# Performance work log

Measured on AMD Instinct MI355X. Metric: run time of the kernel, lower is better.

Reference implementation:

```python
import jax, jax.numpy as jnp
import numpy as np

B, V, D = 8, 1024, 512
H = 8
HD = D // H
MAX_HOP = 8


def setup_inputs() -> dict:
    key = jax.random.key(0)
    ks = jax.random.split(key, 5)
    x = jax.random.normal(ks[0], (B, V, D), dtype=jnp.float32)
    w_qkv = jax.random.normal(ks[1], (D, 3 * D), dtype=jnp.float32) * (D ** -0.5)
    w_out = jax.random.normal(ks[2], (D, D), dtype=jnp.float32) * (D ** -0.5)
    b_out = jnp.zeros((D,), dtype=jnp.float32)
    rpe_bias = jax.random.normal(ks[3], (H, MAX_HOP + 1), dtype=jnp.float32) * 0.02
    hop_matrix = jax.random.randint(ks[4], (V, V), 0, MAX_HOP + 1, dtype=jnp.int32)
    return {"x": x, "w_qkv": w_qkv, "w_out": w_out, "b_out": b_out,
            "rpe_bias": rpe_bias, "hop_matrix": hop_matrix}


def reference(x, w_qkv, w_out, b_out, rpe_bias, hop_matrix):
    b, v, d = x.shape
    scale = HD ** -0.5
    qkv = x @ w_qkv                                   # [B, V, 3D]
    q, k, val = jnp.split(qkv, 3, axis=-1)
    # [B, V, D] -> [B, H, V, HD]
    def split_heads(t):
        return t.reshape(b, v, H, HD).transpose(0, 2, 1, 3)
    q, k, val = split_heads(q), split_heads(k), split_heads(val)
    scores = jnp.einsum('bhvd,bhwd->bhvw', q, k)      # [B, H, V, V]
    bias = rpe_bias[:, hop_matrix]                    # gather -> [H, V, V]
    attn = jax.nn.softmax((scores + bias[None]) * scale, axis=-1)
    out_heads = jnp.einsum('bhvw,bhwd->bhvd', attn, val)
    out = out_heads.transpose(0, 2, 1, 3).reshape(b, v, d)
    out = out @ w_out + b_out
    return out, attn
```

## Files before the change

### kernel.cpp

```cpp
#include <hip/hip_runtime.h>

typedef __attribute__((ext_vector_type(8))) short bf16x8;
typedef __attribute__((ext_vector_type(4))) float f32x4;

#define MFMA16(A,B,C) __builtin_amdgcn_mfma_f32_16x16x32_bf16(A,B,C,0,0,0)

typedef const __attribute__((address_space(1))) void gas_t;
typedef __attribute__((address_space(3))) void las_t;
#define GLOAD16(g, l) __builtin_amdgcn_global_load_lds((gas_t*)(g), (las_t*)(l), 16, 0, 0)

__device__ __forceinline__ unsigned short f2bf(float f){
  unsigned int u = __float_as_uint(f);
  u += 0x7FFFu + ((u >> 16) & 1u);
  return (unsigned short)(u >> 16);
}
__device__ __forceinline__ float bf2f(unsigned short s){
  return __uint_as_float(((unsigned int)s) << 16);
}
__device__ __forceinline__ int swz(int row, int kbyte){
  return (row * 128 + kbyte) ^ ((row & 7) << 4);
}

__global__ __launch_bounds__(256) void k_prep(
    const float* __restrict__ w_qkv, const float* __restrict__ w_out,
    const float* __restrict__ x,
    const int* __restrict__ hop, const float* __restrict__ rpe_bias,
    unsigned short* __restrict__ wqT, unsigned short* __restrict__ woT,
    unsigned short* __restrict__ xb, unsigned short* __restrict__ biasT)
{
  __shared__ float tile[64][65];
  __shared__ float rl[72];
  const int bid = blockIdx.x, tid = threadIdx.x;
  if (bid < 256) {
    const float* src; unsigned short* dst; int srcld, kq0, n0;
    if (bid < 192) {
      int tn = bid >> 3, tk = bid & 7;
      src = w_qkv; dst = wqT; srcld = 1536; kq0 = tk * 64; n0 = tn * 64;
    } else {
      int j = bid - 192; int tn = j >> 3, tk = j & 7;
      src = w_out; dst = woT; srcld = 512; kq0 = tk * 64; n0 = tn * 64;
    }
    const int c = tid & 63, r4 = tid >> 6;
#pragma unroll
    for (int i = 0; i < 16; ++i) {
      int rr = r4 * 16 + i;
      tile[rr][c] = src[(size_t)(kq0 + rr) * srcld + n0 + c];
    }
    __syncthreads();
#pragma unroll
    for (int i = 0; i < 16; ++i) {
      int rr = r4 * 16 + i;
      dst[(size_t)(n0 + rr) * 512 + kq0 + c] = f2bf(tile[c][rr]);
    }
  } else if (bid < 1280) {
    int base = (bid - 256) * 1024 + tid;
#pragma unroll
    for (int i = 0; i < 4; ++i) {
      int j = base + i * 256;
      float4 xv = *reinterpret_cast<const float4*>(x + (size_t)j * 4);
      ushort4 o;
      o.x = f2bf(xv.x); o.y = f2bf(xv.y); o.z = f2bf(xv.z); o.w = f2bf(xv.w);
      *reinterpret_cast<ushort4*>(xb + (size_t)j * 4) = o;
    }
  } else {
    if (tid < 72) rl[tid] = rpe_bias[tid];
    __syncthreads();
    int j = (bid - 1280) * 256 + tid;
    int hv = hop[j];
#pragma unroll
    for (int h = 0; h < 8; ++h)
      biasT[((size_t)h << 20) + j] = f2bf(rl[h * 9 + hv]);
  }
}

__global__ __launch_bounds__(256) void k_qkv(
    const unsigned short* __restrict__ xb, const unsigned short* __restrict__ wqT,
    unsigned short* __restrict__ q, unsigned short* __restrict__ k_,
    unsigned short* __restrict__ valT)
{
  __shared__ char lds[32768];
  char* At = lds; char* Bt = lds + 16384;
  const int tid = threadIdx.x;
  const int wid = tid >> 6, lane = tid & 63, g = lane >> 4, r = lane & 15;
  const int wm = wid >> 1, wn = wid & 1;
  const int m0 = blockIdx.x * 128, n0 = blockIdx.y * 128;
  const int l8 = lane >> 3;
  const int colel = ((lane & 7) ^ l8) * 8;

  f32x4 acc[4][4];
#pragma unroll
  for (int a = 0; a < 4; ++a)
#pragma unroll
    for (int b = 0; b < 4; ++b) acc[a][b] = (f32x4){0.f, 0.f, 0.f, 0.f};

  for (int kt = 0; kt < 8; ++kt) {
    const int k0 = kt * 64;
    __syncthreads();
#pragma unroll
    for (int i = 0; i < 4; ++i) {
      int row = wid * 32 + i * 8 + l8;
      GLOAD16(xb  + (size_t)(m0 + row) * 512 + k0 + colel, At + wid * 4096 + i * 1024);
      GLOAD16(wqT + (size_t)(n0 + row) * 512 + k0 + colel, Bt + wid * 4096 + i * 1024);
    }
    __syncthreads();
#pragma unroll
    for (int kk = 0; kk < 2; ++kk) {
      bf16x8 af[4], bf[4];
      const int kb = (kk * 32 + 8 * g) * 2;
#pragma unroll
      for (int mi = 0; mi < 4; ++mi)
        af[mi] = *reinterpret_cast<const bf16x8*>(At + swz(wm * 64 + mi * 16 + r, kb));
#pragma unroll
      for (int ni = 0; ni < 4; ++ni)
        bf[ni] = *reinterpret_cast<const bf16x8*>(Bt + swz(wn * 64 + ni * 16 + r, kb));
#pragma unroll
      for (int mi = 0; mi < 4; ++mi)
#pragma unroll
        for (int ni = 0; ni < 4; ++ni)
          acc[mi][ni] = MFMA16(af[mi], bf[ni], acc[mi][ni]);
    }
  }
  const int s = n0 >> 9;
#pragma unroll
  for (int mi = 0; mi < 4; ++mi)
#pragma unroll
    for (int ni = 0; ni < 4; ++ni)
#pragma unroll
      for (int i = 0; i < 4; ++i) {
        int m = m0 + wm * 64 + mi * 16 + 4 * g + i;
        int n = n0 + wn * 64 + ni * 16 + r;
        int b = m >> 10, v = m & 1023;
        int cc = n & 511, h = cc >> 6, d = cc & 63;
        int bh = b * 8 + h;
        unsigned short bfv = f2bf(acc[mi][ni][i]);
        if (s == 2)      valT[((size_t)bh * 64 + d) * 1024 + v] = bfv;
        else if (s == 0) q [((size_t)bh * 1024 + v) * 64 + d] = bfv;
        else             k_[((size_t)bh * 1024 + v) * 64 + d] = bfv;
      }
}

#define PSTR 1032
__global__ __launch_bounds__(256, 4) void k_attn(
    const unsigned short* __restrict__ q, const unsigned short* __restrict__ k_,
    const unsigned short* __restrict__ valT,
    const unsigned short* __restrict__ biasT,
    float* __restrict__ attn, unsigned short* __restrict__ oh)
{
  __shared__ unsigned short P[16 * PSTR];
  __shared__ float red[2][4][16];
  const int tid = threadIdx.x;
  const int wid = tid >> 6, lane = tid & 63, g = lane >> 4, r = lane & 15;
  const int blk = ((blockIdx.x & 7) << 9) | (blockIdx.x >> 3);
  const int h  = blk >> 9;
  const int vt = (blk >> 3) & 63;
  const int b  = blk & 7;
  const int bh = b * 8 + h;
  const int v0 = vt * 16;

  const unsigned short* bb = biasT + ((size_t)h << 20) + (size_t)v0 * 1024;
#pragma unroll
  for (int it = 0; it < 8; ++it) {
    int e = tid + it * 256;
    int row = e >> 7, c8 = e & 127;
    *reinterpret_cast<uint4*>(&P[row * PSTR + c8 * 8]) =
        *reinterpret_cast<const uint4*>(bb + (size_t)row * 1024 + c8 * 8);
  }

  const unsigned short* qp = q + ((size_t)bh * 1024 + v0) * 64;
  bf16x8 qf[2];
#pragma unroll
  for (int kk = 0; kk < 2; ++kk)
    qf[kk] = *reinterpret_cast<const bf16x8*>(qp + r * 64 + kk * 32 + 8 * g);
  __syncthreads();

  const unsigned short* kb = k_ + (size_t)bh * 65536;
  f32x4 s[16];
#pragma unroll
  for (int ct = 0; ct < 16; ++ct) {
    const int wcol = wid * 256 + ct * 16 + r;
    f32x4 acc = (f32x4){0.f, 0.f, 0.f, 0.f};
#pragma unroll
    for (int kk = 0; kk < 2; ++kk) {
      bf16x8 kf = *reinterpret_cast<const bf16x8*>(kb + (size_t)wcol * 64 + kk * 32 + 8 * g);
      acc = MFMA16(qf[kk], kf, acc);
    }
#pragma unroll
    for (int i = 0; i < 4; ++i)
      s[ct][i] = (acc[i] + bf2f(P[(4 * g + i) * PSTR + wcol])) * 0.125f;
  }

  float mx[4] = {-1e30f, -1e30f, -1e30f, -1e30f};
#pragma unroll
  for (int ct = 0; ct < 16; ++ct)
#pragma unroll
    for (int i = 0; i < 4; ++i) mx[i] = fmaxf(mx[i], s[ct][i]);
#pragma unroll
  for (int o = 1; o <= 8; o <<= 1)
#pragma unroll
    for (int i = 0; i < 4; ++i) mx[i] = fmaxf(mx[i], __shfl_xor(mx[i], o, 64));
  if (r == 0)
#pragma unroll
    for (int i = 0; i < 4; ++i) red[0][wid][4 * g + i] = mx[i];
  __syncthreads();
#pragma unroll
  for (int i = 0; i < 4; ++i) {
    float M = red[0][0][4 * g + i];
#pragma unroll
    for (int w = 1; w < 4; ++w) M = fmaxf(M, red[0][w][4 * g + i]);
    mx[i] = M;
  }

  float sm[4] = {0.f, 0.f, 0.f, 0.f};
#pragma unroll
  for (int ct = 0; ct < 16; ++ct)
#pragma unroll
    for (int i = 0; i < 4; ++i) {
      float e = __expf(s[ct][i] - mx[i]);
      s[ct][i] = e;
      sm[i] += e;
    }
#pragma unroll
  for (int o = 1; o <= 8; o <<= 1)
#pragma unroll
    for (int i = 0; i < 4; ++i) sm[i] += __shfl_xor(sm[i], o, 64);
  if (r == 0)
#pragma unroll
    for (int i = 0; i < 4; ++i) red[1][wid][4 * g + i] = sm[i];
  __syncthreads();
  float inv[4];
#pragma unroll
  for (int i = 0; i < 4; ++i) {
    float T = red[1][0][4 * g + i] + red[1][1][4 * g + i] +
              red[1][2][4 * g + i] + red[1][3][4 * g + i];
    inv[i] = 1.0f / T;
  }

#pragma unroll
  for (int ct = 0; ct < 16; ++ct) {
    const int col = wid * 256 + ct * 16 + r;
#pragma unroll
    for (int i = 0; i < 4; ++i)
      P[(4 * g + i) * PSTR + col] = f2bf(s[ct][i] * inv[i]);
  }
  __syncthreads();

  float* ab = attn + ((size_t)bh * 1024 + v0) * 1024;
#pragma unroll
  for (int it = 0; it < 16; ++it) {
    int e = tid + it * 256;
    int row = e >> 8, q4 = e & 255;
    uint2 pv = *reinterpret_cast<const uint2*>(&P[row * PSTR + q4 * 4]);
    f32x4 o;
    o[0] = bf2f((unsigned short)(pv.x      ));
    o[1] = bf2f((unsigned short)(pv.x >> 16));
    o[2] = bf2f((unsigned short)(pv.y      ));
    o[3] = bf2f((unsigned short)(pv.y >> 16));
    __builtin_nontemporal_store(o, reinterpret_cast<f32x4*>(ab + (size_t)row * 1024 + q4 * 4));
  }

  const unsigned short* vT = valT + ((size_t)bh * 64 + wid * 16) * 1024;
  f32x4 a0 = (f32x4){0.f,0.f,0.f,0.f}, a1 = a0;
  for (int kc = 0; kc < 32; kc += 2) {
    const int base = r * PSTR, vbase = kc * 32 + 8 * g;
    bf16x8 p0 = *reinterpret_cast<const bf16x8*>(&P[base + vbase]);
    bf16x8 p1 = *reinterpret_cast<const bf16x8*>(&P[base + vbase + 32]);
    bf16x8 v0_ = *reinterpret_cast<const bf16x8*>(vT + (size_t)r * 1024 + vbase);
    bf16x8 v1_ = *reinterpret_cast<const bf16x8*>(vT + (size_t)r * 1024 + vbase + 32);
    a0 = MFMA16(p0, v0_, a0);
    a1 = MFMA16(p1, v1_, a1);
  }
  f32x4 acc = a0 + a1;
#pragma unroll
  for (int i = 0; i < 4; ++i) {
    size_t oi = ((size_t)(b * 1024 + v0 + 4 * g + i)) * 512 + h * 64 + wid * 16 + r;
    oh[oi] = f2bf(acc[i]);
  }
}

__global__ __launch_bounds__(256) void k_out(
    const unsigned short* __restrict__ oh, const unsigned short* __restrict__ woT,
    const float* __restrict__ b_out, float* __restrict__ out)
{
  __shared__ char lds[32768];
  char* At = lds; char* Bt = lds + 16384;
  const int tid = threadIdx.x;
  const int wid = tid >> 6, lane = tid & 63, g = lane >> 4, r = lane & 15;
  const int wm = wid >> 1, wn = wid & 1;
  const int m0 = blockIdx.x * 128, n0 = blockIdx.y * 128;
  const int l8 = lane >> 3;
  const int colel = ((lane & 7) ^ l8) * 8;

  f32x4 acc[4][4];
#pragma unroll
  for (int a = 0; a < 4; ++a)
#pragma unroll
    for (int b = 0; b < 4; ++b) acc[a][b] = (f32x4){0.f, 0.f, 0.f, 0.f};

  for (int kt = 0; kt < 8; ++kt) {
    const int k0 = kt * 64;
    __syncthreads();
#pragma unroll
    for (int i = 0; i < 4; ++i) {
      int row = wid * 32 + i * 8 + l8;
      GLOAD16(oh  + (size_t)(m0 + row) * 512 + k0 + colel, At + wid * 4096 + i * 1024);
      GLOAD16(woT + (size_t)(n0 + row) * 512 + k0 + colel, Bt + wid * 4096 + i * 1024);
    }
    __syncthreads();
#pragma unroll
    for (int kk = 0; kk < 2; ++kk) {
      bf16x8 a4[4], b4[4];
      const int kb = (kk * 32 + 8 * g) * 2;
#pragma unroll
      for (int mi = 0; mi < 4; ++mi)
        a4[mi] = *reinterpret_cast<const bf16x8*>(At + swz(wm * 64 + mi * 16 + r, kb));
#pragma unroll
      for (int ni = 0; ni < 4; ++ni)
        b4[ni] = *reinterpret_cast<const bf16x8*>(Bt + swz(wn * 64 + ni * 16 + r, kb));
#pragma unroll
      for (int mi = 0; mi < 4; ++mi)
#pragma unroll
        for (int ni = 0; ni < 4; ++ni)
          acc[mi][ni] = MFMA16(a4[mi], b4[ni], acc[mi][ni]);
    }
  }
#pragma unroll
  for (int mi = 0; mi < 4; ++mi)
#pragma unroll
    for (int ni = 0; ni < 4; ++ni)
#pragma unroll
      for (int i = 0; i < 4; ++i) {
        int m = m0 + wm * 64 + mi * 16 + 4 * g + i;
        int n = n0 + wn * 64 + ni * 16 + r;
        float v = acc[mi][ni][i] + b_out[n];
        __builtin_nontemporal_store(v, out + (size_t)m * 512 + n);
      }
}

extern "C" void kernel_launch(void* const* d_in, const int* in_sizes, int n_in,
                              void* d_out, int out_size, void* d_ws, size_t ws_size,
                              hipStream_t stream) {
  const float *x = nullptr, *w_qkv = nullptr, *w_out = nullptr,
              *b_out = nullptr, *rpe = nullptr;
  const int* hop = nullptr;
  for (int i = 0; i < n_in; ++i) {
    switch (in_sizes[i]) {
      case 4194304: x     = (const float*)d_in[i]; break;
      case 786432:  w_qkv = (const float*)d_in[i]; break;
      case 262144:  w_out = (const float*)d_in[i]; break;
      case 512:     b_out = (const float*)d_in[i]; break;
      case 72:      rpe   = (const float*)d_in[i]; break;
      case 1048576: hop   = (const int*)d_in[i];   break;
    }
  }

  float* out  = (float*)d_out;
  float* attn = out + (size_t)4194304;

  char* ws = (char*)d_ws;
  unsigned short* q_    = (unsigned short*)(ws);
  unsigned short* k_    = (unsigned short*)(ws + (size_t) 8388608);
  unsigned short* valT  = (unsigned short*)(ws + (size_t)16777216);
  unsigned short* oh    = (unsigned short*)(ws + (size_t)25165824);
  unsigned short* wqT   = (unsigned short*)(ws + (size_t)33554432);
  unsigned short* woT   = (unsigned short*)(ws + (size_t)35127296);
  unsigned short* biasT = (unsigned short*)(ws + (size_t)35651584);
  unsigned short* xb    = (unsigned short*)(ws + (size_t)52428800);

  k_prep<<<dim3(5376), dim3(256), 0, stream>>>(w_qkv, w_out, x, hop, rpe,
                                               wqT, woT, xb, biasT);
  k_qkv<<<dim3(64, 12), dim3(256), 0, stream>>>(xb, wqT, q_, k_, valT);
  k_attn<<<dim3(4096), dim3(256), 0, stream>>>(q_, k_, valT, biasT, attn, oh);
  k_out<<<dim3(64, 4), dim3(256), 0, stream>>>(oh, woT, b_out, out);
}
```

Before: 194.0 us.

## Replace precomputed per-head bf16 bias with transposed uint8 hop lookup in attention

The prep kernel no longer expands the relative-position bias into an [H,V,V] bf16 tensor. It writes a transposed uint8 copy of the hop matrix instead. The attention kernel loads the 9 per-head rpe values into shared memory and adds them per score by indexing with the packed hop bytes. This removes a 16 MB bias write and most of the bias read traffic. In exchange it adds strided 4-byte global loads per column tile and per-lane LDS lookups with possible bank conflicts.

```diff
diff --git a/kernel.cpp b/kernel.cpp
--- a/kernel.cpp
+++ b/kernel.cpp
@@ -23,14 +23,14 @@
 
 __global__ __launch_bounds__(256) void k_prep(
     const float* __restrict__ w_qkv, const float* __restrict__ w_out,
-    const float* __restrict__ x,
-    const int* __restrict__ hop, const float* __restrict__ rpe_bias,
+    const float* __restrict__ x, const int* __restrict__ hop,
     unsigned short* __restrict__ wqT, unsigned short* __restrict__ woT,
-    unsigned short* __restrict__ xb, unsigned short* __restrict__ biasT)
+    unsigned short* __restrict__ xb, unsigned char* __restrict__ hop8T)
 {
   __shared__ float tile[64][65];
-  __shared__ float rl[72];
+  __shared__ int itile[64][65];
   const int bid = blockIdx.x, tid = threadIdx.x;
+  const int c = tid & 63, r4 = tid >> 6;
   if (bid < 256) {
     const float* src; unsigned short* dst; int srcld, kq0, n0;
     if (bid < 192) {
@@ -40,7 +40,6 @@
       int j = bid - 192; int tn = j >> 3, tk = j & 7;
       src = w_out; dst = woT; srcld = 512; kq0 = tk * 64; n0 = tn * 64;
     }
-    const int c = tid & 63, r4 = tid >> 6;
 #pragma unroll
     for (int i = 0; i < 16; ++i) {
       int rr = r4 * 16 + i;
@@ -52,8 +51,22 @@
       int rr = r4 * 16 + i;
       dst[(size_t)(n0 + rr) * 512 + kq0 + c] = f2bf(tile[c][rr]);
     }
-  } else if (bid < 1280) {
-    int base = (bid - 256) * 1024 + tid;
+  } else if (bid < 512) {
+    int j = bid - 256; int tv = j >> 4, tw = j & 15;
+#pragma unroll
+    for (int i = 0; i < 16; ++i) {
+      int rr = r4 * 16 + i;
+      itile[rr][c] = hop[(size_t)(tv * 64 + rr) * 1024 + tw * 64 + c];
+    }
+    __syncthreads();
+#pragma unroll
+    for (int i = 0; i < 16; ++i) {
+      int rr = r4 * 16 + i;
+      hop8T[(size_t)(tw * 64 + rr) * 1024 + tv * 64 + c] =
+          (unsigned char)itile[c][rr];
+    }
+  } else {
+    int base = (bid - 512) * 1024 + tid;
 #pragma unroll
     for (int i = 0; i < 4; ++i) {
       int j = base + i * 256;
@@ -62,14 +75,6 @@
       o.x = f2bf(xv.x); o.y = f2bf(xv.y); o.z = f2bf(xv.z); o.w = f2bf(xv.w);
       *reinterpret_cast<ushort4*>(xb + (size_t)j * 4) = o;
     }
-  } else {
-    if (tid < 72) rl[tid] = rpe_bias[tid];
-    __syncthreads();
-    int j = (bid - 1280) * 256 + tid;
-    int hv = hop[j];
-#pragma unroll
-    for (int h = 0; h < 8; ++h)
-      biasT[((size_t)h << 20) + j] = f2bf(rl[h * 9 + hv]);
   }
 }
 
@@ -143,11 +148,13 @@
 __global__ __launch_bounds__(256, 4) void k_attn(
     const unsigned short* __restrict__ q, const unsigned short* __restrict__ k_,
     const unsigned short* __restrict__ valT,
-    const unsigned short* __restrict__ biasT,
+    const unsigned char* __restrict__ hop8T,
+    const float* __restrict__ rpe_bias,
     float* __restrict__ attn, unsigned short* __restrict__ oh)
 {
   __shared__ unsigned short P[16 * PSTR];
   __shared__ float red[2][4][16];
+  __shared__ float rl[9];
   const int tid = threadIdx.x;
   const int wid = tid >> 6, lane = tid & 63, g = lane >> 4, r = lane & 15;
   const int blk = ((blockIdx.x & 7) << 9) | (blockIdx.x >> 3);
@@ -157,14 +164,7 @@
   const int bh = b * 8 + h;
   const int v0 = vt * 16;
 
-  const unsigned short* bb = biasT + ((size_t)h << 20) + (size_t)v0 * 1024;
-#pragma unroll
-  for (int it = 0; it < 8; ++it) {
-    int e = tid + it * 256;
-    int row = e >> 7, c8 = e & 127;
-    *reinterpret_cast<uint4*>(&P[row * PSTR + c8 * 8]) =
-        *reinterpret_cast<const uint4*>(bb + (size_t)row * 1024 + c8 * 8);
-  }
+  if (tid < 9) rl[tid] = rpe_bias[h * 9 + tid];
 
   const unsigned short* qp = q + ((size_t)bh * 1024 + v0) * 64;
   bf16x8 qf[2];
@@ -178,6 +178,8 @@
 #pragma unroll
   for (int ct = 0; ct < 16; ++ct) {
     const int wcol = wid * 256 + ct * 16 + r;
+    unsigned int hv = *reinterpret_cast<const unsigned int*>(
+        hop8T + (size_t)wcol * 1024 + v0 + 4 * g);
     f32x4 acc = (f32x4){0.f, 0.f, 0.f, 0.f};
 #pragma unroll
     for (int kk = 0; kk < 2; ++kk) {
@@ -186,7 +188,7 @@
     }
 #pragma unroll
     for (int i = 0; i < 4; ++i)
-      s[ct][i] = (acc[i] + bf2f(P[(4 * g + i) * PSTR + wcol])) * 0.125f;
+      s[ct][i] = (acc[i] + rl[(hv >> (8 * i)) & 0xFF]) * 0.125f;
   }
 
   float mx[4] = {-1e30f, -1e30f, -1e30f, -1e30f};
@@ -363,12 +365,12 @@
   unsigned short* oh    = (unsigned short*)(ws + (size_t)25165824);
   unsigned short* wqT   = (unsigned short*)(ws + (size_t)33554432);
   unsigned short* woT   = (unsigned short*)(ws + (size_t)35127296);
-  unsigned short* biasT = (unsigned short*)(ws + (size_t)35651584);
+  unsigned char*  hop8T = (unsigned char*)(ws + (size_t)35651584);
   unsigned short* xb    = (unsigned short*)(ws + (size_t)52428800);
 
-  k_prep<<<dim3(5376), dim3(256), 0, stream>>>(w_qkv, w_out, x, hop, rpe,
-                                               wqT, woT, xb, biasT);
+  k_prep<<<dim3(1536), dim3(256), 0, stream>>>(w_qkv, w_out, x, hop,
+                                               wqT, woT, xb, hop8T);
   k_qkv<<<dim3(64, 12), dim3(256), 0, stream>>>(xb, wqT, q_, k_, valT);
-  k_attn<<<dim3(4096), dim3(256), 0, stream>>>(q_, k_, valT, biasT, attn, oh);
+  k_attn<<<dim3(4096), dim3(256), 0, stream>>>(q_, k_, valT, hop8T, rpe, attn, oh);
   k_out<<<dim3(64, 4), dim3(256), 0, stream>>>(oh, woT, b_out, out);
 }
```

Result: slower. 211.9 us (+9.3%).
